# Optimization experiments

Hardware: AMD Instinct MI355X
Metric: run time of the kernel (lower is better)

Reference implementation:

```python
import jax, jax.numpy as jnp
import numpy as np

BN_EPS = 1e-5

def batchnorm(x, gamma, beta):
    # training-mode BN over axis 0 with biased variance (matches torch)
    mean = jnp.mean(x, axis=0)
    var = jnp.var(x, axis=0)
    return (x - mean) * jax.lax.rsqrt(var + BN_EPS) * gamma + beta

def setup_inputs() -> dict:
    key = jax.random.key(0)
    ks = jax.random.split(key, 8)
    N, M, A, B = 50000, 12, 64, 41
    atom_in_fea = jax.random.normal(ks[0], (N, A), dtype=jnp.float32)
    nbr_fea = jax.random.normal(ks[1], (N, M, B), dtype=jnp.float32)
    nbr_fea_idx = jax.random.randint(ks[2], (N, M), 0, N)
    fan_in = 2 * A + B
    lim = 1.0 / np.sqrt(fan_in)
    W = jax.random.uniform(ks[3], (2 * A, fan_in), minval=-lim, maxval=lim, dtype=jnp.float32)
    b = jax.random.uniform(ks[4], (2 * A,), minval=-lim, maxval=lim, dtype=jnp.float32)
    bn1_g = jnp.ones((2 * A,), jnp.float32)
    bn1_b = jnp.zeros((2 * A,), jnp.float32)
    bn2_g = jnp.ones((A,), jnp.float32)
    bn2_b = jnp.zeros((A,), jnp.float32)
    return {"atom_in_fea": atom_in_fea, "nbr_fea": nbr_fea, "nbr_fea_idx": nbr_fea_idx,
            "W": W, "b": b, "bn1_g": bn1_g, "bn1_b": bn1_b, "bn2_g": bn2_g, "bn2_b": bn2_b}

def reference(atom_in_fea, nbr_fea, nbr_fea_idx, W, b, bn1_g, bn1_b, bn2_g, bn2_b):
    N, M = nbr_fea_idx.shape
    A = atom_in_fea.shape[1]
    atom_nbr_fea = atom_in_fea[nbr_fea_idx]                       # (N, M, A) gather
    self_fea = jnp.broadcast_to(atom_in_fea[:, None, :], (N, M, A))
    total_nbr_fea = jnp.concatenate([self_fea, atom_nbr_fea, nbr_fea], axis=2)  # (N,M,2A+B)
    total_gated = jnp.einsum('nmf,of->nmo', total_nbr_fea, W) + b  # (N,M,2A)
    total_gated = batchnorm(total_gated.reshape(-1, 2 * A), bn1_g, bn1_b).reshape(N, M, 2 * A)
    nbr_filter, nbr_core = total_gated[..., :A], total_gated[..., A:]
    nbr_sumed = jnp.sum(jax.nn.sigmoid(nbr_filter) * jax.nn.softplus(nbr_core), axis=1)  # (N,A)
    nbr_sumed = batchnorm(nbr_sumed, bn2_g, bn2_b)
    return jax.nn.softplus(atom_in_fea + nbr_sumed)
```

## Files before the change

kernel.cpp:

```cpp
#include <hip/hip_runtime.h>
#include <math.h>

#define N_ATOMS 50000
#define M_NBR   12
#define A_FEA   64
#define B_FEA   41
#define KF      169
#define KP      192
#define LDA     200
#define OC      128
#define NROW    600000
#define TR32    32
#define NT32    18750
#define NT192   3125
#define BN_EPS  1e-5f
#define L2E     1.44269504088896340736f
#define LN2     0.693147180559945309417f

#define WS_SUM1   0
#define WS_SUMSQ1 128
#define WS_SUM2   256
#define WS_SUMSQ2 320
#define WS_NFLOAT 384
#define WS_GATED_OFF 2048ull
#define GATED_BYTES  ((size_t)NT32 * 512 * 16)

#define BAR_LGKM() asm volatile("s_waitcnt lgkmcnt(0)\n\ts_barrier" ::: "memory")

typedef __attribute__((ext_vector_type(8))) short s16x8;
typedef __attribute__((ext_vector_type(4))) float f32x4;

__device__ __forceinline__ float fsigmoid(float x) {
    float e = __builtin_amdgcn_exp2f(-x * L2E);
    return __builtin_amdgcn_rcpf(1.f + e);
}
__device__ __forceinline__ float fsoftplus(float x) {
    float e = __builtin_amdgcn_exp2f(-fabsf(x) * L2E);
    return fmaxf(x, 0.f) + __builtin_amdgcn_logf(1.f + e) * LN2;
}
__device__ __forceinline__ unsigned int pack2bf(float lo, float hi) {
    unsigned int r;
    asm("v_cvt_pk_bf16_f32 %0, %1, %2" : "=v"(r) : "v"(lo), "v"(hi));
    return r;
}
__device__ __forceinline__ unsigned short f2bf(float f) {
    unsigned int r;
    asm("v_cvt_pk_bf16_f32 %0, %1, %1" : "=v"(r) : "v"(f));
    return (unsigned short)r;
}
__device__ __forceinline__ float bf_lo(unsigned int u) { return __uint_as_float(u << 16); }
__device__ __forceinline__ float bf_hi(unsigned int u) { return __uint_as_float(u & 0xFFFF0000u); }

__global__ void k_zero_stats(float* __restrict__ stats) {
    int i = blockIdx.x * blockDim.x + threadIdx.x;
    if (i < WS_NFLOAT) stats[i] = 0.f;
}
__global__ void k_zero(float* __restrict__ dout, float* __restrict__ stats) {
    int i = blockIdx.x * blockDim.x + threadIdx.x;
    int stride = gridDim.x * blockDim.x;
    for (int j = i; j < N_ATOMS * A_FEA; j += stride) dout[j] = 0.f;
    if (i < WS_NFLOAT) stats[i] = 0.f;
}

struct TileRegs {
    float4 selfv[2];
    float4 gat[2];
    float4 bond0, bond1;
};

__device__ __forceinline__ void issue_selfbond(TileRegs& R, const float* __restrict__ atom,
                                               const float* __restrict__ nbr,
                                               int rb, int r16, int k4, int tid) {
#pragma unroll
    for (int it = 0; it < 2; ++it) {
        int row = rb + r16 + it * 16;
        R.selfv[it] = *(const float4*)(atom + ((unsigned)row / 12u) * A_FEA + k4);
    }
    const float* bb = nbr + (size_t)rb * B_FEA;
    R.bond0 = *(const float4*)(bb + (size_t)tid * 4);
    if (tid < 72) R.bond1 = *(const float4*)(bb + (size_t)(256 + tid) * 4);
}
__device__ __forceinline__ void issue_gat(TileRegs& R, const float* __restrict__ atom,
                                          const int nbi[2], int k4) {
#pragma unroll
    for (int it = 0; it < 2; ++it)
        R.gat[it] = *(const float4*)(atom + (unsigned)nbi[it] * A_FEA + k4);
}
__device__ __forceinline__ void write_tile(unsigned short* __restrict__ At,
                                           const TileRegs& R, int r16, int k4, int tid) {
#pragma unroll
    for (int it = 0; it < 2; ++it) {
        int r = r16 + it * 16;
        uint2 u;
        u.x = pack2bf(R.selfv[it].x, R.selfv[it].y);
        u.y = pack2bf(R.selfv[it].z, R.selfv[it].w);
        *(uint2*)&At[r * LDA + k4] = u;
        uint2 v;
        v.x = pack2bf(R.gat[it].x, R.gat[it].y);
        v.y = pack2bf(R.gat[it].z, R.gat[it].w);
        *(uint2*)&At[r * LDA + A_FEA + k4] = v;
    }
    {
        const float bv[4] = {R.bond0.x, R.bond0.y, R.bond0.z, R.bond0.w};
#pragma unroll
        for (int e = 0; e < 4; ++e) {
            int le = tid * 4 + e;
            unsigned r = (unsigned)le / 41u, j = (unsigned)le - r * 41u;
            At[r * LDA + 2 * A_FEA + j] = f2bf(bv[e]);
        }
    }
    if (tid < 72) {
        const float bv[4] = {R.bond1.x, R.bond1.y, R.bond1.z, R.bond1.w};
#pragma unroll
        for (int e = 0; e < 4; ++e) {
            int le = 1024 + tid * 4 + e;
            unsigned r = (unsigned)le / 41u, j = (unsigned)le - r * 41u;
            At[r * LDA + 2 * A_FEA + j] = f2bf(bv[e]);
        }
    }
}

template <bool STORE>
__global__ __launch_bounds__(256, 3)
void k_gemm_spill(const float* __restrict__ atom, const float* __restrict__ nbr,
                  const int* __restrict__ idx, const float* __restrict__ W,
                  float* __restrict__ stats, uint4* __restrict__ gated) {
    __shared__ __align__(16) unsigned short At[2][TR32 * LDA];
    const int tid = threadIdx.x;
    for (int i = tid; i < 2 * TR32 * (KP - KF); i += 256) {
        int b  = i / (TR32 * (KP - KF));
        int ii = i - b * (TR32 * (KP - KF));
        int r  = ii / (KP - KF);
        int j  = KF + ii - r * (KP - KF);
        At[b][r * LDA + j] = 0;
    }
    const int lane = tid & 63, gg = tid >> 6;
    const int col  = lane & 15, q8 = (lane >> 4) * 8;
    const int r16  = tid >> 4;
    const int k4   = (tid & 15) * 4;

    s16x8 bfr[2][6];
#pragma unroll
    for (int tt = 0; tt < 2; ++tt) {
        const float* wr = W + ((gg + tt * 4) * 16 + col) * KF;
#pragma unroll
        for (int kc = 0; kc < 6; ++kc) {
            int kb = kc * 32 + q8;
            s16x8 f;
#pragma unroll
            for (int j = 0; j < 8; ++j) {
                int k = kb + j;
                f[j] = (short)f2bf(k < KF ? wr[k] : 0.f);
            }
            bfr[tt][kc] = f;
        }
    }

    const int base = NT32 / gridDim.x;
    const int rem  = NT32 % gridDim.x;
    const int bid  = blockIdx.x;
    const int tA   = bid * base + min(bid, rem);
    const int tB   = tA + base + (bid < rem ? 1 : 0);

    float s[2] = {0.f, 0.f}, q[2] = {0.f, 0.f};
    TileRegs R;
    int nbiN[2];
    if (tA < tB) {
        int rb = tA * TR32;
        int nbiC[2] = {idx[rb + r16], idx[rb + r16 + 16]};
        issue_selfbond(R, atom, nbr, rb, r16, k4, tid);
        issue_gat(R, atom, nbiC, k4);
        if (tA + 1 < tB) {
            int rb1 = rb + TR32;
            nbiN[0] = idx[rb1 + r16]; nbiN[1] = idx[rb1 + r16 + 16];
        }
    }
    int p = 0;
    for (int t = tA; t < tB; ++t) {
        write_tile(At[p], R, r16, k4, tid);
        if (t + 1 < tB) {
            issue_selfbond(R, atom, nbr, (t + 1) * TR32, r16, k4, tid);
            issue_gat(R, atom, nbiN, k4);
            if (t + 2 < tB) {
                int rb2 = (t + 2) * TR32;
                nbiN[0] = idx[rb2 + r16]; nbiN[1] = idx[rb2 + r16 + 16];
            }
        }
        BAR_LGKM();
        const unsigned short* A = At[p];
        f32x4 acc[2][2];
#pragma unroll
        for (int rt = 0; rt < 2; ++rt)
#pragma unroll
            for (int tt = 0; tt < 2; ++tt) acc[rt][tt] = (f32x4){0.f, 0.f, 0.f, 0.f};
#pragma unroll
        for (int kc = 0; kc < 6; ++kc) {
            const int k0 = kc * 32;
            const s16x8 a0 = *(const s16x8*)&A[(col) * LDA + k0 + q8];
            const s16x8 a1 = *(const s16x8*)&A[(16 + col) * LDA + k0 + q8];
#pragma unroll
            for (int tt = 0; tt < 2; ++tt) {
                acc[0][tt] = __builtin_amdgcn_mfma_f32_16x16x32_bf16(a0, bfr[tt][kc], acc[0][tt], 0, 0, 0);
                acc[1][tt] = __builtin_amdgcn_mfma_f32_16x16x32_bf16(a1, bfr[tt][kc], acc[1][tt], 0, 0, 0);
            }
        }
#pragma unroll
        for (int tt = 0; tt < 2; ++tt)
#pragma unroll
            for (int rt = 0; rt < 2; ++rt)
#pragma unroll
                for (int e = 0; e < 4; ++e) {
                    float v = acc[rt][tt][e];
                    s[tt] += v; q[tt] = fmaf(v, v, q[tt]);
                }
        if (STORE) {
#pragma unroll
            for (int rt = 0; rt < 2; ++rt) {
                uint4 u;
                u.x = pack2bf(acc[rt][0][0], acc[rt][0][1]);
                u.y = pack2bf(acc[rt][0][2], acc[rt][0][3]);
                u.z = pack2bf(acc[rt][1][0], acc[rt][1][1]);
                u.w = pack2bf(acc[rt][1][2], acc[rt][1][3]);
                gated[(size_t)t * 512 + rt * 256 + tid] = u;
            }
        }
        p ^= 1;
    }
#pragma unroll
    for (int tt = 0; tt < 2; ++tt) {
        float sv = s[tt], qv = q[tt];
        sv += __shfl_xor(sv, 16); sv += __shfl_xor(sv, 32);
        qv += __shfl_xor(qv, 16); qv += __shfl_xor(qv, 32);
        if (lane < 16) {
            int c = (gg + tt * 4) * 16 + col;
            atomicAdd(&stats[WS_SUM1 + c], sv);
            atomicAdd(&stats[WS_SUMSQ1 + c], qv);
        }
    }
}

__global__ __launch_bounds__(256, 3)
void k_apply(const uint4* __restrict__ gated,
             const float* __restrict__ g1, const float* __restrict__ b1,
             float* __restrict__ stats, float* __restrict__ dout) {
    __shared__ float red[512];
    const int tid = threadIdx.x;
    const int c   = tid & 63;
    const int w   = tid >> 6;
    const int col = c & 15, gg = c >> 4;

    const float invn = 1.f / (float)NROW;
    float meanF = stats[WS_SUM1 + c] * invn;
    float varF  = stats[WS_SUMSQ1 + c] * invn - meanF * meanF;
    float scF   = g1[c] * rsqrtf(varF + BN_EPS), shF = b1[c] - meanF * scF;
    const int cc = c + 64;
    float meanC = stats[WS_SUM1 + cc] * invn;
    float varC  = stats[WS_SUMSQ1 + cc] * invn - meanC * meanC;
    float scC   = g1[cc] * rsqrtf(varC + BN_EPS), shC = b1[cc] - meanC * scC;

    float bs = 0.f, bq = 0.f;
    for (int T = blockIdx.x; T < NT192; T += gridDim.x) {
        uint4 G[4][3];
#pragma unroll
        for (int j = 0; j < 4; ++j) {
            const int a = j * 4 + w;
#pragma unroll
            for (int l = 0; l < 3; ++l) {
                const int Gi  = 3 * a + l;
                const int sub = Gi >> 3, rt = (Gi >> 2) & 1, q = Gi & 3;
                G[j][l] = gated[(size_t)(T * 6 + sub) * 512 + rt * 256
                                + gg * 64 + q * 16 + col];
            }
        }
#pragma unroll
        for (int j = 0; j < 4; ++j) {
            float sum = 0.f;
#pragma unroll
            for (int l = 0; l < 3; ++l) {
                const uint4 u = G[j][l];
                const float fv[4] = {bf_lo(u.x), bf_hi(u.x), bf_lo(u.y), bf_hi(u.y)};
                const float cv[4] = {bf_lo(u.z), bf_hi(u.z), bf_lo(u.w), bf_hi(u.w)};
#pragma unroll
                for (int e = 0; e < 4; ++e) {
                    float gF = fmaf(fv[e], scF, shF);
                    float gC = fmaf(cv[e], scC, shC);
                    sum += fsigmoid(gF) * fsoftplus(gC);
                }
            }
            const int a = j * 4 + w;
            dout[((size_t)T * 16 + a) * 64 + c] = sum;
            bs += sum; bq = fmaf(sum, sum, bq);
        }
    }
    red[tid] = bs; red[256 + tid] = bq;
    __syncthreads();
    if (tid < 64) {
        float ss = red[tid] + red[tid + 64] + red[tid + 128] + red[tid + 192];
        float qq = red[256 + tid] + red[256 + tid + 64] + red[256 + tid + 128] + red[256 + tid + 192];
        atomicAdd(&stats[WS_SUM2 + tid], ss);
        atomicAdd(&stats[WS_SUMSQ2 + tid], qq);
    }
}

__global__ __launch_bounds__(256, 2)
void k_gemm_main(const float* __restrict__ atom, const float* __restrict__ nbr,
                 const int* __restrict__ idx, const float* __restrict__ W,
                 const float* __restrict__ g1, const float* __restrict__ b1,
                 const float* __restrict__ stats, float* __restrict__ dout) {
    __shared__ __align__(16) unsigned short At[TR32 * LDA];
    __shared__ float S[4 * 64];
    const int tid = threadIdx.x;
    for (int i = tid; i < TR32 * (KP - KF); i += 256) {
        int r = i / (KP - KF), j = KF + i - r * (KP - KF);
        At[r * LDA + j] = 0;
    }
    for (int i = tid; i < 4 * 64; i += 256) S[i] = 0.f;
    const int lane = tid & 63, gg = tid >> 6;
    const int col = lane & 15, q8 = (lane >> 4) * 8, quad = lane >> 4;
    const int r16 = tid >> 4, k4 = (tid & 15) * 4;

    s16x8 bfr[2][6];
#pragma unroll
    for (int tt = 0; tt < 2; ++tt) {
        const float* wr = W + ((gg + tt * 4) * 16 + col) * KF;
#pragma unroll
        for (int kc = 0; kc < 6; ++kc) {
            int kb = kc * 32 + q8;
            s16x8 f;
#pragma unroll
            for (int j = 0; j < 8; ++j) { int k = kb + j; f[j] = (short)f2bf(k < KF ? wr[k] : 0.f); }
            bfr[tt][kc] = f;
        }
    }
    const float invn = 1.f / (float)NROW;
    float sc[2], sh[2];
#pragma unroll
    for (int tt = 0; tt < 2; ++tt) {
        int c = (gg + tt * 4) * 16 + col;
        float mean = stats[WS_SUM1 + c] * invn;
        float var  = stats[WS_SUMSQ1 + c] * invn - mean * mean;
        sc[tt] = g1[c] * rsqrtf(var + BN_EPS);
        sh[tt] = b1[c] - mean * sc[tt];
    }
    const int per = (NT32 + gridDim.x - 1) / gridDim.x;
    const int tA = blockIdx.x * per, tB = min(NT32, tA + per);
    for (int t = tA; t < tB; ++t) {
        const int rb = t * TR32;
        __syncthreads();
        {
            TileRegs R;
            int nbiC[2] = {idx[rb + r16], idx[rb + r16 + 16]};
            issue_selfbond(R, atom, nbr, rb, r16, k4, tid);
            issue_gat(R, atom, nbiC, k4);
            write_tile(At, R, r16, k4, tid);
        }
        __syncthreads();
        f32x4 acc[2][2];
#pragma unroll
        for (int rt = 0; rt < 2; ++rt)
#pragma unroll
            for (int tt = 0; tt < 2; ++tt) acc[rt][tt] = (f32x4){0.f, 0.f, 0.f, 0.f};
#pragma unroll
        for (int kc = 0; kc < 6; ++kc) {
            const int k0 = kc * 32;
            const s16x8 a0 = *(const s16x8*)&At[(col) * LDA + k0 + q8];
            const s16x8 a1 = *(const s16x8*)&At[(16 + col) * LDA + k0 + q8];
#pragma unroll
            for (int tt = 0; tt < 2; ++tt) {
                acc[0][tt] = __builtin_amdgcn_mfma_f32_16x16x32_bf16(a0, bfr[tt][kc], acc[0][tt], 0, 0, 0);
                acc[1][tt] = __builtin_amdgcn_mfma_f32_16x16x32_bf16(a1, bfr[tt][kc], acc[1][tt], 0, 0, 0);
            }
        }
        const int a0i = rb / M_NBR;
#pragma unroll
        for (int rt = 0; rt < 2; ++rt)
#pragma unroll
            for (int e = 0; e < 4; ++e) {
                float gF = fmaf(acc[rt][0][e], sc[0], sh[0]);
                float gC = fmaf(acc[rt][1][e], sc[1], sh[1]);
                float v  = fsigmoid(gF) * fsoftplus(gC);
                int row = rb + rt * 16 + quad * 4 + e;
                atomicAdd(&S[(row / M_NBR - a0i) * 64 + gg * 16 + col], v);
            }
        __syncthreads();
        const int amax = (rb + TR32 - 1) / M_NBR - a0i;
        for (int i = tid; i < 4 * 64; i += 256) {
            float v = S[i];
            S[i] = 0.f;
            int a = i >> 6;
            if (a <= amax) atomicAdd(&dout[(a0i + a) * 64 + (i & 63)], v);
        }
    }
}

__global__ __launch_bounds__(256, 1)
void k_bn2_stats(const float* __restrict__ dout, float* __restrict__ stats) {
    int tid = threadIdx.x;
    int c = tid & 63;
    int g = tid >> 6;
    float s = 0.f, q = 0.f;
    for (int n = blockIdx.x * 4 + g; n < N_ATOMS; n += gridDim.x * 4) {
        float v = dout[n * 64 + c];
        s += v; q = fmaf(v, v, q);
    }
    __shared__ float red[4][64];
    red[g][c] = s;
    __syncthreads();
    if (g == 0)
        atomicAdd(&stats[WS_SUM2 + c], red[0][c] + red[1][c] + red[2][c] + red[3][c]);
    __syncthreads();
    red[g][c] = q;
    __syncthreads();
    if (g == 0)
        atomicAdd(&stats[WS_SUMSQ2 + c], red[0][c] + red[1][c] + red[2][c] + red[3][c]);
}

__global__ void k_final(const float* __restrict__ atom, const float* __restrict__ g2,
                        const float* __restrict__ b2, const float* __restrict__ stats,
                        float* __restrict__ dout) {
    int i0 = blockIdx.x * blockDim.x + threadIdx.x;
    int c = i0 & 63;
    const float invn = 1.f / (float)N_ATOMS;
    float mean = stats[WS_SUM2 + c] * invn;
    float var  = stats[WS_SUMSQ2 + c] * invn - mean * mean;
    float sc   = g2[c] * rsqrtf(var + BN_EPS);
    float sh   = b2[c] - mean * sc;
    int stride = gridDim.x * blockDim.x;
    for (int i = i0; i < N_ATOMS * A_FEA; i += stride) {
        float v = fmaf(dout[i], sc, sh) + atom[i];
        dout[i] = fsoftplus(v);
    }
}

extern "C" void kernel_launch(void* const* d_in, const int* in_sizes, int n_in,
                              void* d_out, int out_size, void* d_ws, size_t ws_size,
                              hipStream_t stream) {
    const float* atom = (const float*)d_in[0];
    const float* nbr  = (const float*)d_in[1];
    const int*   idx  = (const int*)d_in[2];
    const float* W    = (const float*)d_in[3];
    const float* g1   = (const float*)d_in[5];
    const float* b1   = (const float*)d_in[6];
    const float* g2   = (const float*)d_in[7];
    const float* b2   = (const float*)d_in[8];
    float* dout  = (float*)d_out;
    float* stats = (float*)d_ws;
    uint4* gated = (uint4*)((char*)d_ws + WS_GATED_OFF);

    const bool fused = ws_size >= (WS_GATED_OFF + GATED_BYTES);

    if (fused) {
        k_zero_stats<<<2, 256, 0, stream>>>(stats);
        k_gemm_spill<true><<<750, 256, 0, stream>>>(atom, nbr, idx, W, stats, gated);
        k_apply<<<625, 256, 0, stream>>>(gated, g1, b1, stats, dout);
        k_final<<<512, 256, 0, stream>>>(atom, g2, b2, stats, dout);
    } else {
        k_zero<<<512, 256, 0, stream>>>(dout, stats);
        k_gemm_spill<false><<<750, 256, 0, stream>>>(atom, nbr, idx, W, stats, nullptr);
        k_gemm_main<<<1024, 256, 0, stream>>>(atom, nbr, idx, W, g1, b1, stats, dout);
        k_bn2_stats<<<256, 256, 0, stream>>>(dout, stats);
        k_final<<<512, 256, 0, stream>>>(atom, g2, b2, stats, dout);
    }
}
```

Measured before the change: 258.8 us.

## Fuse four-kernel pipeline into one cooperative kernel with grid syncs

Replaces the separate zero-stats, GEMM-spill, BN1-apply and final kernels with a single cooperative kernel of 750 blocks that uses grid.sync between phases. This removes three kernel launch boundaries and their gaps. The apply and final phases now run with 750 blocks instead of 625/512, and every phase pays grid-wide barrier costs. The old multi-kernel path is kept as a fallback if the cooperative launch fails.

```diff
diff --git a/kernel.cpp b/kernel.cpp
--- a/kernel.cpp
+++ b/kernel.cpp
@@ -1,5 +1,8 @@
 #include <hip/hip_runtime.h>
+#include <hip/hip_cooperative_groups.h>
 #include <math.h>
+
+namespace cg = cooperative_groups;
 
 #define N_ATOMS 50000
 #define M_NBR   12
@@ -120,6 +123,215 @@
     }
 }
 
+__global__ __launch_bounds__(256, 3)
+void k_fused(const float* __restrict__ atom, const float* __restrict__ nbr,
+             const int* __restrict__ idx, const float* __restrict__ W,
+             const float* __restrict__ g1, const float* __restrict__ b1,
+             const float* __restrict__ g2, const float* __restrict__ b2,
+             float* __restrict__ stats, uint4* __restrict__ gated,
+             float* __restrict__ dout) {
+    cg::grid_group grid = cg::this_grid();
+    __shared__ __align__(16) unsigned short At[2][TR32 * LDA];
+    const int tid = threadIdx.x;
+
+    if (blockIdx.x < 2) {
+        int i = blockIdx.x * 256 + tid;
+        if (i < WS_NFLOAT) stats[i] = 0.f;
+    }
+    __threadfence();
+    grid.sync();
+
+    {
+        for (int i = tid; i < 2 * TR32 * (KP - KF); i += 256) {
+            int b  = i / (TR32 * (KP - KF));
+            int ii = i - b * (TR32 * (KP - KF));
+            int r  = ii / (KP - KF);
+            int j  = KF + ii - r * (KP - KF);
+            At[b][r * LDA + j] = 0;
+        }
+        const int lane = tid & 63, gg = tid >> 6;
+        const int col  = lane & 15, q8 = (lane >> 4) * 8;
+        const int r16  = tid >> 4;
+        const int k4   = (tid & 15) * 4;
+
+        s16x8 bfr[2][6];
+#pragma unroll
+        for (int tt = 0; tt < 2; ++tt) {
+            const float* wr = W + ((gg + tt * 4) * 16 + col) * KF;
+#pragma unroll
+            for (int kc = 0; kc < 6; ++kc) {
+                int kb = kc * 32 + q8;
+                s16x8 f;
+#pragma unroll
+                for (int j = 0; j < 8; ++j) {
+                    int k = kb + j;
+                    f[j] = (short)f2bf(k < KF ? wr[k] : 0.f);
+                }
+                bfr[tt][kc] = f;
+            }
+        }
+
+        const int base = NT32 / gridDim.x;
+        const int rem  = NT32 % gridDim.x;
+        const int bid  = blockIdx.x;
+        const int tA   = bid * base + min(bid, rem);
+        const int tB   = tA + base + (bid < rem ? 1 : 0);
+
+        float s[2] = {0.f, 0.f}, q[2] = {0.f, 0.f};
+        TileRegs R;
+        int nbiN[2];
+        if (tA < tB) {
+            int rb = tA * TR32;
+            int nbiC[2] = {idx[rb + r16], idx[rb + r16 + 16]};
+            issue_selfbond(R, atom, nbr, rb, r16, k4, tid);
+            issue_gat(R, atom, nbiC, k4);
+            if (tA + 1 < tB) {
+                int rb1 = rb + TR32;
+                nbiN[0] = idx[rb1 + r16]; nbiN[1] = idx[rb1 + r16 + 16];
+            }
+        }
+        int p = 0;
+        for (int t = tA; t < tB; ++t) {
+            write_tile(At[p], R, r16, k4, tid);
+            if (t + 1 < tB) {
+                issue_selfbond(R, atom, nbr, (t + 1) * TR32, r16, k4, tid);
+                issue_gat(R, atom, nbiN, k4);
+                if (t + 2 < tB) {
+                    int rb2 = (t + 2) * TR32;
+                    nbiN[0] = idx[rb2 + r16]; nbiN[1] = idx[rb2 + r16 + 16];
+                }
+            }
+            BAR_LGKM();
+            const unsigned short* A = At[p];
+            f32x4 acc[2][2];
+#pragma unroll
+            for (int rt = 0; rt < 2; ++rt)
+#pragma unroll
+                for (int tt = 0; tt < 2; ++tt) acc[rt][tt] = (f32x4){0.f, 0.f, 0.f, 0.f};
+#pragma unroll
+            for (int kc = 0; kc < 6; ++kc) {
+                const int k0 = kc * 32;
+                const s16x8 a0 = *(const s16x8*)&A[(col) * LDA + k0 + q8];
+                const s16x8 a1 = *(const s16x8*)&A[(16 + col) * LDA + k0 + q8];
+#pragma unroll
+                for (int tt = 0; tt < 2; ++tt) {
+                    acc[0][tt] = __builtin_amdgcn_mfma_f32_16x16x32_bf16(a0, bfr[tt][kc], acc[0][tt], 0, 0, 0);
+                    acc[1][tt] = __builtin_amdgcn_mfma_f32_16x16x32_bf16(a1, bfr[tt][kc], acc[1][tt], 0, 0, 0);
+                }
+            }
+#pragma unroll
+            for (int tt = 0; tt < 2; ++tt)
+#pragma unroll
+                for (int rt = 0; rt < 2; ++rt)
+#pragma unroll
+                    for (int e = 0; e < 4; ++e) {
+                        float v = acc[rt][tt][e];
+                        s[tt] += v; q[tt] = fmaf(v, v, q[tt]);
+                    }
+#pragma unroll
+            for (int rt = 0; rt < 2; ++rt) {
+                uint4 u;
+                u.x = pack2bf(acc[rt][0][0], acc[rt][0][1]);
+                u.y = pack2bf(acc[rt][0][2], acc[rt][0][3]);
+                u.z = pack2bf(acc[rt][1][0], acc[rt][1][1]);
+                u.w = pack2bf(acc[rt][1][2], acc[rt][1][3]);
+                gated[(size_t)t * 512 + rt * 256 + tid] = u;
+            }
+            p ^= 1;
+        }
+#pragma unroll
+        for (int tt = 0; tt < 2; ++tt) {
+            float sv = s[tt], qv = q[tt];
+            sv += __shfl_xor(sv, 16); sv += __shfl_xor(sv, 32);
+            qv += __shfl_xor(qv, 16); qv += __shfl_xor(qv, 32);
+            if (lane < 16) {
+                int c = (gg + tt * 4) * 16 + col;
+                atomicAdd(&stats[WS_SUM1 + c], sv);
+                atomicAdd(&stats[WS_SUMSQ1 + c], qv);
+            }
+        }
+    }
+    __threadfence();
+    grid.sync();
+
+    {
+        float* red = (float*)&At[0][0];
+        const int c   = tid & 63;
+        const int w   = tid >> 6;
+        const int col = c & 15, gg = c >> 4;
+
+        const float invn = 1.f / (float)NROW;
+        float meanF = stats[WS_SUM1 + c] * invn;
+        float varF  = stats[WS_SUMSQ1 + c] * invn - meanF * meanF;
+        float scF   = g1[c] * rsqrtf(varF + BN_EPS), shF = b1[c] - meanF * scF;
+        const int cc = c + 64;
+        float meanC = stats[WS_SUM1 + cc] * invn;
+        float varC  = stats[WS_SUMSQ1 + cc] * invn - meanC * meanC;
+        float scC   = g1[cc] * rsqrtf(varC + BN_EPS), shC = b1[cc] - meanC * scC;
+
+        float bs = 0.f, bq = 0.f;
+        for (int T = blockIdx.x; T < NT192; T += gridDim.x) {
+            uint4 G[4][3];
+#pragma unroll
+            for (int j = 0; j < 4; ++j) {
+                const int a = j * 4 + w;
+#pragma unroll
+                for (int l = 0; l < 3; ++l) {
+                    const int Gi  = 3 * a + l;
+                    const int sub = Gi >> 3, rt = (Gi >> 2) & 1, qq = Gi & 3;
+                    G[j][l] = gated[(size_t)(T * 6 + sub) * 512 + rt * 256
+                                    + gg * 64 + qq * 16 + col];
+                }
+            }
+#pragma unroll
+            for (int j = 0; j < 4; ++j) {
+                float sum = 0.f;
+#pragma unroll
+                for (int l = 0; l < 3; ++l) {
+                    const uint4 u = G[j][l];
+                    const float fv[4] = {bf_lo(u.x), bf_hi(u.x), bf_lo(u.y), bf_hi(u.y)};
+                    const float cv[4] = {bf_lo(u.z), bf_hi(u.z), bf_lo(u.w), bf_hi(u.w)};
+#pragma unroll
+                    for (int e = 0; e < 4; ++e) {
+                        float gF = fmaf(fv[e], scF, shF);
+                        float gC = fmaf(cv[e], scC, shC);
+                        sum += fsigmoid(gF) * fsoftplus(gC);
+                    }
+                }
+                const int a = j * 4 + w;
+                dout[((size_t)T * 16 + a) * 64 + c] = sum;
+                bs += sum; bq = fmaf(sum, sum, bq);
+            }
+        }
+        __syncthreads();
+        red[tid] = bs; red[256 + tid] = bq;
+        __syncthreads();
+        if (tid < 64) {
+            float ss = red[tid] + red[tid + 64] + red[tid + 128] + red[tid + 192];
+            float qq = red[256 + tid] + red[256 + tid + 64] + red[256 + tid + 128] + red[256 + tid + 192];
+            atomicAdd(&stats[WS_SUM2 + tid], ss);
+            atomicAdd(&stats[WS_SUMSQ2 + tid], qq);
+        }
+    }
+    __threadfence();
+    grid.sync();
+
+    {
+        const int i0 = blockIdx.x * 256 + tid;
+        const int c = i0 & 63;
+        const float invn = 1.f / (float)N_ATOMS;
+        float mean = stats[WS_SUM2 + c] * invn;
+        float var  = stats[WS_SUMSQ2 + c] * invn - mean * mean;
+        float sc   = g2[c] * rsqrtf(var + BN_EPS);
+        float sh   = b2[c] - mean * sc;
+        const int stride = gridDim.x * 256;
+        for (int i = i0; i < N_ATOMS * A_FEA; i += stride) {
+            float v = fmaf(dout[i], sc, sh) + atom[i];
+            dout[i] = fsoftplus(v);
+        }
+    }
+}
+
 template <bool STORE>
 __global__ __launch_bounds__(256, 3)
 void k_gemm_spill(const float* __restrict__ atom, const float* __restrict__ nbr,
@@ -155,7 +367,6 @@
             bfr[tt][kc] = f;
         }
     }
-
     const int base = NT32 / gridDim.x;
     const int rem  = NT32 % gridDim.x;
     const int bid  = blockIdx.x;
@@ -450,10 +661,18 @@
     const bool fused = ws_size >= (WS_GATED_OFF + GATED_BYTES);
 
     if (fused) {
-        k_zero_stats<<<2, 256, 0, stream>>>(stats);
-        k_gemm_spill<true><<<750, 256, 0, stream>>>(atom, nbr, idx, W, stats, gated);
-        k_apply<<<625, 256, 0, stream>>>(gated, g1, b1, stats, dout);
-        k_final<<<512, 256, 0, stream>>>(atom, g2, b2, stats, dout);
+        void* args[] = {(void*)&atom, (void*)&nbr, (void*)&idx, (void*)&W,
+                        (void*)&g1, (void*)&b1, (void*)&g2, (void*)&b2,
+                        (void*)&stats, (void*)&gated, (void*)&dout};
+        hipError_t err = hipLaunchCooperativeKernel((const void*)k_fused,
+                                                    dim3(750), dim3(256),
+                                                    args, 0, stream);
+        if (err != hipSuccess) {
+            k_zero_stats<<<2, 256, 0, stream>>>(stats);
+            k_gemm_spill<true><<<750, 256, 0, stream>>>(atom, nbr, idx, W, stats, gated);
+            k_apply<<<625, 256, 0, stream>>>(gated, g1, b1, stats, dout);
+            k_final<<<512, 256, 0, stream>>>(atom, g2, b2, stats, dout);
+        }
     } else {
         k_zero<<<512, 256, 0, stream>>>(dout, stats);
         k_gemm_spill<false><<<750, 256, 0, stream>>>(atom, nbr, idx, W, stats, nullptr);
```

Result: slower. 696.1 us (+169.0%).

## Grow GEMM row tile to 64 with a single LDS buffer

Applied to the files above, without the earlier changes.

The fused gather+GEMM kernel now processes 64-row tiles instead of 32, issuing four row groups of MFMAs per K chunk against the register-resident weight fragments. The LDS tile is single-buffered, so a second barrier per tile is added to protect reuse. Stores remap so that each 64-row tile still writes two 32-row gated slots in the same layout. The aim is to amortise barriers and loop overhead over more MFMA work per tile. In exchange it holds more prefetch registers and adds an extra barrier that can serialise LDS writes with compute.

```diff
diff --git a/kernel.cpp b/kernel.cpp
--- a/kernel.cpp
+++ b/kernel.cpp
@@ -11,7 +11,9 @@
 #define OC      128
 #define NROW    600000
 #define TR32    32
+#define TR64    64
 #define NT32    18750
+#define NT64    9375
 #define NT192   3125
 #define BN_EPS  1e-5f
 #define L2E     1.44269504088896340736f
@@ -67,7 +69,6 @@
     float4 gat[2];
     float4 bond0, bond1;
 };
-
 __device__ __forceinline__ void issue_selfbond(TileRegs& R, const float* __restrict__ atom,
                                                const float* __restrict__ nbr,
                                                int rb, int r16, int k4, int tid) {
@@ -120,19 +121,84 @@
     }
 }
 
+struct TileRegs64 {
+    float4 selfv[4];
+    float4 gat[4];
+    float4 bond0, bond1, bond2;
+};
+__device__ __forceinline__ void issue_selfbond64(TileRegs64& R, const float* __restrict__ atom,
+                                                 const float* __restrict__ nbr,
+                                                 int rb, int r16, int k4, int tid) {
+#pragma unroll
+    for (int it = 0; it < 4; ++it) {
+        int row = rb + r16 + it * 16;
+        R.selfv[it] = *(const float4*)(atom + ((unsigned)row / 12u) * A_FEA + k4);
+    }
+    const float* bb = nbr + (size_t)rb * B_FEA;
+    R.bond0 = *(const float4*)(bb + (size_t)tid * 4);
+    R.bond1 = *(const float4*)(bb + (size_t)(256 + tid) * 4);
+    if (tid < 144) R.bond2 = *(const float4*)(bb + (size_t)(512 + tid) * 4);
+}
+__device__ __forceinline__ void issue_gat64(TileRegs64& R, const float* __restrict__ atom,
+                                            const int nbi[4], int k4) {
+#pragma unroll
+    for (int it = 0; it < 4; ++it)
+        R.gat[it] = *(const float4*)(atom + (unsigned)nbi[it] * A_FEA + k4);
+}
+__device__ __forceinline__ void write_tile64(unsigned short* __restrict__ At,
+                                             const TileRegs64& R, int r16, int k4, int tid) {
+#pragma unroll
+    for (int it = 0; it < 4; ++it) {
+        int r = r16 + it * 16;
+        uint2 u;
+        u.x = pack2bf(R.selfv[it].x, R.selfv[it].y);
+        u.y = pack2bf(R.selfv[it].z, R.selfv[it].w);
+        *(uint2*)&At[r * LDA + k4] = u;
+        uint2 v;
+        v.x = pack2bf(R.gat[it].x, R.gat[it].y);
+        v.y = pack2bf(R.gat[it].z, R.gat[it].w);
+        *(uint2*)&At[r * LDA + A_FEA + k4] = v;
+    }
+    {
+        const float bv[4] = {R.bond0.x, R.bond0.y, R.bond0.z, R.bond0.w};
+#pragma unroll
+        for (int e = 0; e < 4; ++e) {
+            int le = tid * 4 + e;
+            unsigned r = (unsigned)le / 41u, j = (unsigned)le - r * 41u;
+            At[r * LDA + 2 * A_FEA + j] = f2bf(bv[e]);
+        }
+    }
+    {
+        const float bv[4] = {R.bond1.x, R.bond1.y, R.bond1.z, R.bond1.w};
+#pragma unroll
+        for (int e = 0; e < 4; ++e) {
+            int le = 1024 + tid * 4 + e;
+            unsigned r = (unsigned)le / 41u, j = (unsigned)le - r * 41u;
+            At[r * LDA + 2 * A_FEA + j] = f2bf(bv[e]);
+        }
+    }
+    if (tid < 144) {
+        const float bv[4] = {R.bond2.x, R.bond2.y, R.bond2.z, R.bond2.w};
+#pragma unroll
+        for (int e = 0; e < 4; ++e) {
+            int le = 2048 + tid * 4 + e;
+            unsigned r = (unsigned)le / 41u, j = (unsigned)le - r * 41u;
+            At[r * LDA + 2 * A_FEA + j] = f2bf(bv[e]);
+        }
+    }
+}
+
 template <bool STORE>
 __global__ __launch_bounds__(256, 3)
 void k_gemm_spill(const float* __restrict__ atom, const float* __restrict__ nbr,
                   const int* __restrict__ idx, const float* __restrict__ W,
                   float* __restrict__ stats, uint4* __restrict__ gated) {
-    __shared__ __align__(16) unsigned short At[2][TR32 * LDA];
+    __shared__ __align__(16) unsigned short At[TR64 * LDA];
     const int tid = threadIdx.x;
-    for (int i = tid; i < 2 * TR32 * (KP - KF); i += 256) {
-        int b  = i / (TR32 * (KP - KF));
-        int ii = i - b * (TR32 * (KP - KF));
-        int r  = ii / (KP - KF);
-        int j  = KF + ii - r * (KP - KF);
-        At[b][r * LDA + j] = 0;
+    for (int i = tid; i < TR64 * (KP - KF); i += 256) {
+        int r = i / (KP - KF);
+        int j = KF + i - r * (KP - KF);
+        At[r * LDA + j] = 0;
     }
     const int lane = tid & 63, gg = tid >> 6;
     const int col  = lane & 15, q8 = (lane >> 4) * 8;
@@ -156,75 +222,78 @@
         }
     }
 
-    const int base = NT32 / gridDim.x;
-    const int rem  = NT32 % gridDim.x;
+    const int base = NT64 / gridDim.x;
+    const int rem  = NT64 % gridDim.x;
     const int bid  = blockIdx.x;
     const int tA   = bid * base + min(bid, rem);
     const int tB   = tA + base + (bid < rem ? 1 : 0);
 
     float s[2] = {0.f, 0.f}, q[2] = {0.f, 0.f};
-    TileRegs R;
-    int nbiN[2];
+    TileRegs64 R;
+    int nbiN[4];
     if (tA < tB) {
-        int rb = tA * TR32;
-        int nbiC[2] = {idx[rb + r16], idx[rb + r16 + 16]};
-        issue_selfbond(R, atom, nbr, rb, r16, k4, tid);
-        issue_gat(R, atom, nbiC, k4);
+        int rb = tA * TR64;
+        int nb[4];
+#pragma unroll
+        for (int it = 0; it < 4; ++it) nb[it] = idx[rb + r16 + it * 16];
+        issue_selfbond64(R, atom, nbr, rb, r16, k4, tid);
+        issue_gat64(R, atom, nb, k4);
         if (tA + 1 < tB) {
-            int rb1 = rb + TR32;
-            nbiN[0] = idx[rb1 + r16]; nbiN[1] = idx[rb1 + r16 + 16];
-        }
-    }
-    int p = 0;
+            int rb1 = rb + TR64;
+#pragma unroll
+            for (int it = 0; it < 4; ++it) nbiN[it] = idx[rb1 + r16 + it * 16];
+        }
+    }
     for (int t = tA; t < tB; ++t) {
-        write_tile(At[p], R, r16, k4, tid);
+        write_tile64(At, R, r16, k4, tid);
         if (t + 1 < tB) {
-            issue_selfbond(R, atom, nbr, (t + 1) * TR32, r16, k4, tid);
-            issue_gat(R, atom, nbiN, k4);
+            issue_selfbond64(R, atom, nbr, (t + 1) * TR64, r16, k4, tid);
+            issue_gat64(R, atom, nbiN, k4);
             if (t + 2 < tB) {
-                int rb2 = (t + 2) * TR32;
-                nbiN[0] = idx[rb2 + r16]; nbiN[1] = idx[rb2 + r16 + 16];
+                int rb2 = (t + 2) * TR64;
+#pragma unroll
+                for (int it = 0; it < 4; ++it) nbiN[it] = idx[rb2 + r16 + it * 16];
             }
         }
         BAR_LGKM();
-        const unsigned short* A = At[p];
-        f32x4 acc[2][2];
-#pragma unroll
-        for (int rt = 0; rt < 2; ++rt)
-#pragma unroll
-            for (int tt = 0; tt < 2; ++tt) acc[rt][tt] = (f32x4){0.f, 0.f, 0.f, 0.f};
+        f32x4 acc[4][2];
+#pragma unroll
+        for (int rg = 0; rg < 4; ++rg)
+#pragma unroll
+            for (int tt = 0; tt < 2; ++tt) acc[rg][tt] = (f32x4){0.f, 0.f, 0.f, 0.f};
 #pragma unroll
         for (int kc = 0; kc < 6; ++kc) {
             const int k0 = kc * 32;
-            const s16x8 a0 = *(const s16x8*)&A[(col) * LDA + k0 + q8];
-            const s16x8 a1 = *(const s16x8*)&A[(16 + col) * LDA + k0 + q8];
-#pragma unroll
-            for (int tt = 0; tt < 2; ++tt) {
-                acc[0][tt] = __builtin_amdgcn_mfma_f32_16x16x32_bf16(a0, bfr[tt][kc], acc[0][tt], 0, 0, 0);
-                acc[1][tt] = __builtin_amdgcn_mfma_f32_16x16x32_bf16(a1, bfr[tt][kc], acc[1][tt], 0, 0, 0);
+#pragma unroll
+            for (int rg = 0; rg < 4; ++rg) {
+                const s16x8 a = *(const s16x8*)&At[(rg * 16 + col) * LDA + k0 + q8];
+#pragma unroll
+                for (int tt = 0; tt < 2; ++tt)
+                    acc[rg][tt] = __builtin_amdgcn_mfma_f32_16x16x32_bf16(a, bfr[tt][kc], acc[rg][tt], 0, 0, 0);
             }
         }
 #pragma unroll
         for (int tt = 0; tt < 2; ++tt)
 #pragma unroll
-            for (int rt = 0; rt < 2; ++rt)
+            for (int rg = 0; rg < 4; ++rg)
 #pragma unroll
                 for (int e = 0; e < 4; ++e) {
-                    float v = acc[rt][tt][e];
+                    float v = acc[rg][tt][e];
                     s[tt] += v; q[tt] = fmaf(v, v, q[tt]);
                 }
         if (STORE) {
 #pragma unroll
-            for (int rt = 0; rt < 2; ++rt) {
+            for (int rg = 0; rg < 4; ++rg) {
                 uint4 u;
-                u.x = pack2bf(acc[rt][0][0], acc[rt][0][1]);
-                u.y = pack2bf(acc[rt][0][2], acc[rt][0][3]);
-                u.z = pack2bf(acc[rt][1][0], acc[rt][1][1]);
-                u.w = pack2bf(acc[rt][1][2], acc[rt][1][3]);
-                gated[(size_t)t * 512 + rt * 256 + tid] = u;
-            }
-        }
-        p ^= 1;
+                u.x = pack2bf(acc[rg][0][0], acc[rg][0][1]);
+                u.y = pack2bf(acc[rg][0][2], acc[rg][0][3]);
+                u.z = pack2bf(acc[rg][1][0], acc[rg][1][1]);
+                u.w = pack2bf(acc[rg][1][2], acc[rg][1][3]);
+                const int t32 = t * 2 + (rg >> 1);
+                gated[(size_t)t32 * 512 + (rg & 1) * 256 + tid] = u;
+            }
+        }
+        BAR_LGKM();
     }
 #pragma unroll
     for (int tt = 0; tt < 2; ++tt) {
```

Result: slower. 281.7 us (+8.9%).
